# Kernel tuning notes

Hardware: AMD Instinct MI355X
Metric: run time of the kernel (lower is better)

The kernel has to match this reference:

```python
import jax, jax.numpy as jnp
import numpy as np

B, T, E = 1024, 200, 128
H = 64

def setup_inputs() -> dict:
    key = jax.random.key(0)
    k1, k2, k3, k4 = jax.random.split(key, 4)
    return {
        "query": jax.random.normal(k1, (B, 1, E), dtype=jnp.float32),
        "keys": jax.random.normal(k2, (B, T, E), dtype=jnp.float32),
        "W0": jax.random.normal(k3, (4 * E, H), dtype=jnp.float32) * 0.05,
        "b0": jnp.zeros((H,), dtype=jnp.float32),
        "W1": jax.random.normal(k4, (H, 1), dtype=jnp.float32) * 0.05,
        "b1": jnp.zeros((1,), dtype=jnp.float32),
    }

def reference(query, keys, W0, b0, W1, b1):
    # query: [B,1,E] broadcast to [B,T,E] (repeat_elements along axis 1)
    q = jnp.broadcast_to(query, keys.shape)
    # dnn_input: [B,T,4E] = concat([q, k, q-k, q*k])
    x = jnp.concatenate([q, keys, q - keys, q * keys], axis=-1)
    # one hidden layer with relu, then linear scorer -> [B,T,1]
    h = jax.nn.relu(jnp.einsum('btd,dh->bth', x, W0) + b0)
    att_score = jnp.einsum('bth,ho->bto', h, W1) + b1
    return att_score
```

## Files before the change

### kernel.cpp

```cpp
#include <hip/hip_runtime.h>
#include <hip/hip_bf16.h>


#define TB 200
#define EB 128
#define HB 64
#define KROW 136
#define KROWS 208

typedef __attribute__((ext_vector_type(8))) short bf16x8;
typedef __attribute__((ext_vector_type(4))) float f32x4;

__global__ __launch_bounds__(512, 4)
void lau_kernel(const float* __restrict__ query,
                const float* __restrict__ keys,
                const float* __restrict__ W0,
                const float* __restrict__ b0,
                const float* __restrict__ W1,
                const float* __restrict__ b1,
                float* __restrict__ out)
{
    const int b    = blockIdx.x;
    const int tid  = threadIdx.x;
    const int lane = tid & 63;
    const int wave = tid >> 6;
    const int ln15 = lane & 15;
    const int quad = lane >> 4;

    __shared__ float bias_s[HB];
    __shared__ float w1_s[HB];
    __shared__ __align__(16) unsigned char smem[KROWS * KROW * 2];

    float* q_s   = (float*)smem;
    float* red_s = (float*)(smem + 512);
    __hip_bfloat16 (*wbt)[KROW] = (__hip_bfloat16(*)[KROW])(smem + 2560);
    __hip_bfloat16 (*kt)[KROW]  = (__hip_bfloat16(*)[KROW])smem;

    const float* kb = keys + (size_t)b * TB * EB;

    if (tid < EB) q_s[tid] = query[(size_t)b * EB + tid];
    __syncthreads();

    {
        const int h     = tid & 63;
        const int chunk = tid >> 6;
        float biasp = 0.f;
        #pragma unroll 8
        for (int i = 0; i < 16; ++i) {
            const int e = chunk * 16 + i;
            const float qe  = q_s[e];
            const float w0a = W0[(size_t)e            * HB + h];
            const float w0b = W0[(size_t)(EB + e)     * HB + h];
            const float w0c = W0[(size_t)(2 * EB + e) * HB + h];
            const float w0d = W0[(size_t)(3 * EB + e) * HB + h];
            wbt[h][e] = __float2bfloat16(w0b - w0c + qe * w0d);
            biasp += qe * (w0a + w0c);
        }
        red_s[tid] = biasp;
    }
    __syncthreads();
    if (tid < HB) {
        float s = b0[tid];
        #pragma unroll
        for (int j = 0; j < 8; ++j) s += red_s[tid + 64 * j];
        bias_s[tid] = s;
        w1_s[tid]   = W1[tid];
    }
    __syncthreads();

    f32x4 g[7];
    #pragma unroll
    for (int j = 0; j < 7; ++j) {
        const int u = tid + j * 512;
        if (u < 3200) g[j] = __builtin_nontemporal_load((const f32x4*)(kb + (size_t)u * 4));
    }

    bf16x8 wbf[4][4];
    #pragma unroll
    for (int nt = 0; nt < 4; ++nt)
        #pragma unroll
        for (int ks = 0; ks < 4; ++ks)
            wbf[nt][ks] = *(const bf16x8*)&wbt[nt * 16 + ln15][quad * 8 + ks * 32];
    float w1q[4], biasq[4];
    #pragma unroll
    for (int nt = 0; nt < 4; ++nt) {
        w1q[nt]   = w1_s[nt * 16 + ln15];
        biasq[nt] = bias_s[nt * 16 + ln15];
    }

    __syncthreads();

    #pragma unroll
    for (int j = 0; j < 7; ++j) {
        const int u = tid + j * 512;
        if (u < 3200) {
            const int row  = u >> 5;
            const int col4 = (u & 31) * 4;
            union { uint2 w; __hip_bfloat162 h2[2]; } pk;
            pk.h2[0] = __float22bfloat162_rn(make_float2(g[j][0], g[j][1]));
            pk.h2[1] = __float22bfloat162_rn(make_float2(g[j][2], g[j][3]));
            *(uint2*)&kt[row][col4] = pk.w;
        }
    }
    #pragma unroll
    for (int j = 0; j < 7; ++j) {
        const int u = 3200 + tid + j * 512;
        if (u < 6400) g[j] = __builtin_nontemporal_load((const f32x4*)(kb + (size_t)u * 4));
    }
    #pragma unroll
    for (int j = 0; j < 7; ++j) {
        const int u = 3200 + tid + j * 512;
        if (u < 6400) {
            const int row  = u >> 5;
            const int col4 = (u & 31) * 4;
            union { uint2 w; __hip_bfloat162 h2[2]; } pk;
            pk.h2[0] = __float22bfloat162_rn(make_float2(g[j][0], g[j][1]));
            pk.h2[1] = __float22bfloat162_rn(make_float2(g[j][2], g[j][3]));
            *(uint2*)&kt[row][col4] = pk.w;
        }
    }
    __syncthreads();

    const float b1v = b1[0];
    for (int mt = wave; mt < 13; mt += 8) {
        bf16x8 af[4];
        #pragma unroll
        for (int ks = 0; ks < 4; ++ks)
            af[ks] = *(const bf16x8*)&kt[mt * 16 + ln15][quad * 8 + ks * 32];

        f32x4 acc[4] = {{0,0,0,0},{0,0,0,0},{0,0,0,0},{0,0,0,0}};
        #pragma unroll
        for (int ks = 0; ks < 4; ++ks)
            #pragma unroll
            for (int nt = 0; nt < 4; ++nt)
                acc[nt] = __builtin_amdgcn_mfma_f32_16x16x32_bf16(af[ks], wbf[nt][ks], acc[nt], 0, 0, 0);

        float part[4];
        #pragma unroll
        for (int r = 0; r < 4; ++r) {
            float s = 0.f;
            #pragma unroll
            for (int nt = 0; nt < 4; ++nt) {
                float hv = acc[nt][r] + biasq[nt];
                hv = hv > 0.f ? hv : 0.f;
                s += hv * w1q[nt];
            }
            part[r] = s;
        }
        #pragma unroll
        for (int m = 1; m < 16; m <<= 1) {
            #pragma unroll
            for (int r = 0; r < 4; ++r)
                part[r] += __shfl_xor(part[r], m, 64);
        }
        if (ln15 == 0) {
            #pragma unroll
            for (int r = 0; r < 4; ++r) {
                const int mg = mt * 16 + quad * 4 + r;
                if (mg < TB) out[(size_t)b * TB + mg] = part[r] + b1v;
            }
        }
    }
}

extern "C" void kernel_launch(void* const* d_in, const int* in_sizes, int n_in,
                              void* d_out, int out_size, void* d_ws, size_t ws_size,
                              hipStream_t stream) {
    const float* query = (const float*)d_in[0];
    const float* keys  = (const float*)d_in[1];
    const float* W0    = (const float*)d_in[2];
    const float* b0    = (const float*)d_in[3];
    const float* W1    = (const float*)d_in[4];
    const float* b1    = (const float*)d_in[5];
    float* out = (float*)d_out;

    lau_kernel<<<1024, 512, 0, stream>>>(query, keys, W0, b0, W1, b1, out);
}
```

Baseline: 162.8 us.

## Split weight prep into separate kernel and process two batches per block with prefetch

Moves the per-batch folding of W0 into a prep kernel. It writes a batch-independent bf16 weight matrix [W0b-W0c ; W0d] and a per-batch bias to workspace. The main kernel then computes q*k on the fly as a second K=128 MFMA pass, so the contraction grows from 128 to 256. Each block now handles two batches in half-tiles with register prefetch of the next half, which overlaps key loads with MFMA work and shrinks shared memory. The cost is double the MFMA work, a second kernel launch, and reading weight fragments from LDS inside the loop instead of keeping them in registers.

```diff
diff --git a/kernel.cpp b/kernel.cpp
--- a/kernel.cpp
+++ b/kernel.cpp
@@ -6,159 +6,204 @@
 #define EB 128
 #define HB 64
 #define KROW 136
-#define KROWS 208
+#define KT_ROWS 112
+#define WCOL 264
+#define UNITS_B 6400
+#define U_H1 3584
 
 typedef __attribute__((ext_vector_type(8))) short bf16x8;
 typedef __attribute__((ext_vector_type(4))) float f32x4;
 
+__global__ __launch_bounds__(256, 4)
+void prep_kernel(const float* __restrict__ query,
+                 const float* __restrict__ W0,
+                 const float* __restrict__ b0,
+                 unsigned char* __restrict__ ws)
+{
+    const int bid = blockIdx.x, tid = threadIdx.x;
+    __hip_bfloat16* wcat_g = (__hip_bfloat16*)ws;
+    float* bias_g = (float*)(ws + 34048);
+
+    if (bid < 64) {
+        __shared__ float p2s[EB][HB];
+        const int h = tid & 63, ec = tid >> 6;
+        #pragma unroll 4
+        for (int i = 0; i < 32; ++i) {
+            const int e = ec * 32 + i;
+            p2s[e][h] = W0[(size_t)e * HB + h] + W0[(size_t)(2 * EB + e) * HB + h];
+        }
+        __syncthreads();
+        const float b0h = b0[h];
+        for (int pass = 0; pass < 4; ++pass) {
+            const int b = bid * 16 + (tid >> 6) + pass * 4;
+            const float* q = query + (size_t)b * EB;
+            float acc = b0h;
+            #pragma unroll 8
+            for (int e = 0; e < EB; ++e) acc += q[e] * p2s[e][h];
+            bias_g[(size_t)b * HB + h] = acc;
+        }
+    } else {
+        const int h  = tid & 63;
+        const int kc = (bid - 64) * 4 + (tid >> 6);
+        float v;
+        if (kc < 128) v = W0[(size_t)(EB + kc) * HB + h] - W0[(size_t)(2 * EB + kc) * HB + h];
+        else          v = W0[(size_t)(3 * EB + (kc - 128)) * HB + h];
+        wcat_g[(size_t)h * WCOL + kc] = __float2bfloat16(v);
+    }
+}
+
 __global__ __launch_bounds__(512, 4)
-void lau_kernel(const float* __restrict__ query,
-                const float* __restrict__ keys,
-                const float* __restrict__ W0,
-                const float* __restrict__ b0,
-                const float* __restrict__ W1,
-                const float* __restrict__ b1,
-                float* __restrict__ out)
+void lau_main(const float* __restrict__ query,
+              const float* __restrict__ keys,
+              const float* __restrict__ W1,
+              const float* __restrict__ b1,
+              const unsigned char* __restrict__ ws,
+              float* __restrict__ out)
 {
-    const int b    = blockIdx.x;
-    const int tid  = threadIdx.x;
-    const int lane = tid & 63;
-    const int wave = tid >> 6;
-    const int ln15 = lane & 15;
-    const int quad = lane >> 4;
-
+    const int bid  = blockIdx.x, tid = threadIdx.x;
+    const int lane = tid & 63, wave = tid >> 6;
+    const int ln15 = lane & 15, quad = lane >> 4;
+
+    __shared__ __align__(16) __hip_bfloat16 wcat_s[HB][WCOL];
+    __shared__ __align__(16) __hip_bfloat16 kt[KT_ROWS][KROW];
+    __shared__ float q_s[EB];
     __shared__ float bias_s[HB];
     __shared__ float w1_s[HB];
-    __shared__ __align__(16) unsigned char smem[KROWS * KROW * 2];
-
-    float* q_s   = (float*)smem;
-    float* red_s = (float*)(smem + 512);
-    __hip_bfloat16 (*wbt)[KROW] = (__hip_bfloat16(*)[KROW])(smem + 2560);
-    __hip_bfloat16 (*kt)[KROW]  = (__hip_bfloat16(*)[KROW])smem;
-
+
+    const __hip_bfloat16* wcat_g = (const __hip_bfloat16*)ws;
+    const float* bias_g = (const float*)(ws + 34048);
+    const float b1v = b1[0];
+
+    int b = bid * 2;
     const float* kb = keys + (size_t)b * TB * EB;
 
-    if (tid < EB) q_s[tid] = query[(size_t)b * EB + tid];
-    __syncthreads();
+    f32x4 g[7];
+    #pragma unroll
+    for (int j = 0; j < 7; ++j)
+        g[j] = __builtin_nontemporal_load((const f32x4*)(kb + (size_t)(tid + j * 512) * 4));
 
     {
-        const int h     = tid & 63;
-        const int chunk = tid >> 6;
-        float biasp = 0.f;
-        #pragma unroll 8
-        for (int i = 0; i < 16; ++i) {
-            const int e = chunk * 16 + i;
-            const float qe  = q_s[e];
-            const float w0a = W0[(size_t)e            * HB + h];
-            const float w0b = W0[(size_t)(EB + e)     * HB + h];
-            const float w0c = W0[(size_t)(2 * EB + e) * HB + h];
-            const float w0d = W0[(size_t)(3 * EB + e) * HB + h];
-            wbt[h][e] = __float2bfloat16(w0b - w0c + qe * w0d);
-            biasp += qe * (w0a + w0c);
-        }
-        red_s[tid] = biasp;
+        const uint4* src = (const uint4*)wcat_g;
+        uint4* dst = (uint4*)&wcat_s[0][0];
+        #pragma unroll
+        for (int j = 0; j < 4; ++j) dst[tid + j * 512] = src[tid + j * 512];
+        if (tid < 64) dst[2048 + tid] = src[2048 + tid];
+        if (tid < EB) q_s[tid] = query[(size_t)b * EB + tid];
+        if (tid < HB) { bias_s[tid] = bias_g[(size_t)b * HB + tid]; w1_s[tid] = W1[tid]; }
     }
     __syncthreads();
-    if (tid < HB) {
-        float s = b0[tid];
-        #pragma unroll
-        for (int j = 0; j < 8; ++j) s += red_s[tid + 64 * j];
-        bias_s[tid] = s;
-        w1_s[tid]   = W1[tid];
-    }
-    __syncthreads();
-
-    f32x4 g[7];
+
+    float w1q[4];
     #pragma unroll
-    for (int j = 0; j < 7; ++j) {
-        const int u = tid + j * 512;
-        if (u < 3200) g[j] = __builtin_nontemporal_load((const f32x4*)(kb + (size_t)u * 4));
-    }
-
-    bf16x8 wbf[4][4];
-    #pragma unroll
-    for (int nt = 0; nt < 4; ++nt)
+    for (int nt = 0; nt < 4; ++nt) w1q[nt] = w1_s[nt * 16 + ln15];
+
+    float biasq[4];
+
+    auto do_tile = [&](int mt, int lrow) {
+        bf16x8 ak[4];
         #pragma unroll
         for (int ks = 0; ks < 4; ++ks)
-            wbf[nt][ks] = *(const bf16x8*)&wbt[nt * 16 + ln15][quad * 8 + ks * 32];
-    float w1q[4], biasq[4];
-    #pragma unroll
-    for (int nt = 0; nt < 4; ++nt) {
-        w1q[nt]   = w1_s[nt * 16 + ln15];
-        biasq[nt] = bias_s[nt * 16 + ln15];
-    }
-
-    __syncthreads();
-
-    #pragma unroll
-    for (int j = 0; j < 7; ++j) {
-        const int u = tid + j * 512;
-        if (u < 3200) {
-            const int row  = u >> 5;
-            const int col4 = (u & 31) * 4;
+            ak[ks] = *(const bf16x8*)&kt[lrow][quad * 8 + ks * 32];
+        f32x4 acc[4] = {{0,0,0,0},{0,0,0,0},{0,0,0,0},{0,0,0,0}};
+        #pragma unroll
+        for (int ks = 0; ks < 4; ++ks) {
+            #pragma unroll
+            for (int nt = 0; nt < 4; ++nt) {
+                const bf16x8 bf = *(const bf16x8*)&wcat_s[nt * 16 + ln15][quad * 8 + ks * 32];
+                acc[nt] = __builtin_amdgcn_mfma_f32_16x16x32_bf16(ak[ks], bf, acc[nt], 0, 0, 0);
+            }
+        }
+        #pragma unroll
+        for (int ks = 0; ks < 4; ++ks) {
+            union { bf16x8 v; __hip_bfloat162 h2[4]; } kk, qq;
+            kk.v = ak[ks];
+            #pragma unroll
+            for (int j = 0; j < 4; ++j) {
+                const float2 kf = __bfloat1622float2(kk.h2[j]);
+                const int e = quad * 8 + ks * 32 + 2 * j;
+                qq.h2[j] = __float22bfloat162_rn(make_float2(kf.x * q_s[e], kf.y * q_s[e + 1]));
+            }
+            #pragma unroll
+            for (int nt = 0; nt < 4; ++nt) {
+                const bf16x8 bf = *(const bf16x8*)&wcat_s[nt * 16 + ln15][128 + quad * 8 + ks * 32];
+                acc[nt] = __builtin_amdgcn_mfma_f32_16x16x32_bf16(qq.v, bf, acc[nt], 0, 0, 0);
+            }
+        }
+        float part[4];
+        #pragma unroll
+        for (int r = 0; r < 4; ++r) {
+            float s = 0.f;
+            #pragma unroll
+            for (int nt = 0; nt < 4; ++nt) {
+                float hv = acc[nt][r] + biasq[nt];
+                hv = hv > 0.f ? hv : 0.f;
+                s += hv * w1q[nt];
+            }
+            part[r] = s;
+        }
+        #pragma unroll
+        for (int m = 1; m < 16; m <<= 1) {
+            #pragma unroll
+            for (int r = 0; r < 4; ++r) part[r] += __shfl_xor(part[r], m, 64);
+        }
+        if (ln15 == 0) {
+            #pragma unroll
+            for (int r = 0; r < 4; ++r) {
+                const int mg = mt * 16 + quad * 4 + r;
+                if (mg < TB) out[(size_t)b * TB + mg] = part[r] + b1v;
+            }
+        }
+    };
+
+    for (int bt = 0; bt < 2; ++bt) {
+        #pragma unroll
+        for (int j = 0; j < 7; ++j) {
+            const int u = tid + j * 512;
+            const int row = u >> 5, col4 = (u & 31) * 4;
             union { uint2 w; __hip_bfloat162 h2[2]; } pk;
             pk.h2[0] = __float22bfloat162_rn(make_float2(g[j][0], g[j][1]));
             pk.h2[1] = __float22bfloat162_rn(make_float2(g[j][2], g[j][3]));
             *(uint2*)&kt[row][col4] = pk.w;
         }
-    }
-    #pragma unroll
-    for (int j = 0; j < 7; ++j) {
-        const int u = 3200 + tid + j * 512;
-        if (u < 6400) g[j] = __builtin_nontemporal_load((const f32x4*)(kb + (size_t)u * 4));
-    }
-    #pragma unroll
-    for (int j = 0; j < 7; ++j) {
-        const int u = 3200 + tid + j * 512;
-        if (u < 6400) {
-            const int row  = u >> 5;
-            const int col4 = (u & 31) * 4;
+        #pragma unroll
+        for (int j = 0; j < 6; ++j) {
+            int gu = U_H1 + tid + j * 512;
+            gu = gu < UNITS_B ? gu : UNITS_B - 1;
+            g[j] = __builtin_nontemporal_load((const f32x4*)(kb + (size_t)gu * 4));
+        }
+        __syncthreads();
+
+        #pragma unroll
+        for (int nt = 0; nt < 4; ++nt) biasq[nt] = bias_s[nt * 16 + ln15];
+
+        if (wave < 7) do_tile(wave, wave * 16 + ln15);
+        __syncthreads();
+
+        #pragma unroll
+        for (int j = 0; j < 6; ++j) {
+            const int u = tid + j * 512;
+            const int row = u >> 5, col4 = (u & 31) * 4;
             union { uint2 w; __hip_bfloat162 h2[2]; } pk;
             pk.h2[0] = __float22bfloat162_rn(make_float2(g[j][0], g[j][1]));
             pk.h2[1] = __float22bfloat162_rn(make_float2(g[j][2], g[j][3]));
             *(uint2*)&kt[row][col4] = pk.w;
         }
-    }
-    __syncthreads();
-
-    const float b1v = b1[0];
-    for (int mt = wave; mt < 13; mt += 8) {
-        bf16x8 af[4];
-        #pragma unroll
-        for (int ks = 0; ks < 4; ++ks)
-            af[ks] = *(const bf16x8*)&kt[mt * 16 + ln15][quad * 8 + ks * 32];
-
-        f32x4 acc[4] = {{0,0,0,0},{0,0,0,0},{0,0,0,0},{0,0,0,0}};
-        #pragma unroll
-        for (int ks = 0; ks < 4; ++ks)
-            #pragma unroll
-            for (int nt = 0; nt < 4; ++nt)
-                acc[nt] = __builtin_amdgcn_mfma_f32_16x16x32_bf16(af[ks], wbf[nt][ks], acc[nt], 0, 0, 0);
-
-        float part[4];
-        #pragma unroll
-        for (int r = 0; r < 4; ++r) {
-            float s = 0.f;
-            #pragma unroll
-            for (int nt = 0; nt < 4; ++nt) {
-                float hv = acc[nt][r] + biasq[nt];
-                hv = hv > 0.f ? hv : 0.f;
-                s += hv * w1q[nt];
-            }
-            part[r] = s;
-        }
-        #pragma unroll
-        for (int m = 1; m < 16; m <<= 1) {
-            #pragma unroll
-            for (int r = 0; r < 4; ++r)
-                part[r] += __shfl_xor(part[r], m, 64);
-        }
-        if (ln15 == 0) {
-            #pragma unroll
-            for (int r = 0; r < 4; ++r) {
-                const int mg = mt * 16 + quad * 4 + r;
-                if (mg < TB) out[(size_t)b * TB + mg] = part[r] + b1v;
-            }
+        if (bt == 0) {
+            const float* kb1 = keys + (size_t)(b + 1) * TB * EB;
+            #pragma unroll
+            for (int j = 0; j < 7; ++j)
+                g[j] = __builtin_nontemporal_load((const f32x4*)(kb1 + (size_t)(tid + j * 512) * 4));
+        }
+        __syncthreads();
+
+        if (wave < 6) do_tile(7 + wave, (7 + wave) * 16 - 112 + ln15);
+        __syncthreads();
+
+        if (bt == 0) {
+            b += 1;
+            kb = keys + (size_t)b * TB * EB;
+            if (tid < EB) q_s[tid] = query[(size_t)b * EB + tid];
+            if (tid < HB) bias_s[tid] = bias_g[(size_t)b * HB + tid];
         }
     }
 }
@@ -173,6 +218,8 @@
     const float* W1    = (const float*)d_in[4];
     const float* b1    = (const float*)d_in[5];
     float* out = (float*)d_out;
-
-    lau_kernel<<<1024, 512, 0, stream>>>(query, keys, W0, b0, W1, b1, out);
+    unsigned char* ws = (unsigned char*)d_ws;
+
+    prep_kernel<<<128, 256, 0, stream>>>(query, W0, b0, ws);
+    lau_main<<<512, 512, 0, stream>>>(query, keys, W1, b1, ws, out);
 }
```

After: 176.7 us. +8.5%, slower.

## Split per-batch weight folding into a separate prep kernel via workspace

Applied to the files above, without the earlier changes.

Moves the query-dependent folding of W0 into a bf16 weight matrix and bias into a separate prep kernel. Each prep block loads its W0 slice into registers once and reuses it across four batches, writing the results to workspace. The score kernel then reads its folded weights and bias from global memory instead of computing them, which removes the W0 loads and two barriers from its prologue. The cost is an extra launch and about 16 MB of workspace traffic, written by one kernel and read back by the next.

```diff
diff --git a/kernel.cpp b/kernel.cpp
--- a/kernel.cpp
+++ b/kernel.cpp
@@ -7,18 +7,75 @@
 #define HB 64
 #define KROW 136
 #define KROWS 208
+#define WB_BYTES (HB * EB * 2)
+#define BIAS_OFF (1024 * WB_BYTES)
 
 typedef __attribute__((ext_vector_type(8))) short bf16x8;
 typedef __attribute__((ext_vector_type(4))) float f32x4;
 
+__global__ __launch_bounds__(512, 2)
+void prep_kernel(const float* __restrict__ query,
+                 const float* __restrict__ W0,
+                 const float* __restrict__ b0,
+                 unsigned char* __restrict__ ws)
+{
+    const int bid = blockIdx.x, tid = threadIdx.x;
+    const int h     = tid & 63;
+    const int chunk = tid >> 6;
+
+    __shared__ float q_s[4][EB];
+    __shared__ float red_s[512];
+
+    for (int j = tid; j < 4 * EB; j += 512) {
+        const int bb = bid * 4 + (j >> 7);
+        q_s[j >> 7][j & 127] = query[(size_t)bb * EB + (j & 127)];
+    }
+
+    float w0a[16], w0b[16], w0c[16], w0d[16];
+    #pragma unroll
+    for (int i = 0; i < 16; ++i) {
+        const int e = chunk * 16 + i;
+        w0a[i] = W0[(size_t)e            * HB + h];
+        w0b[i] = W0[(size_t)(EB + e)     * HB + h];
+        w0c[i] = W0[(size_t)(2 * EB + e) * HB + h];
+        w0d[i] = W0[(size_t)(3 * EB + e) * HB + h];
+    }
+    __syncthreads();
+
+    const float b0h = b0[h];
+    for (int bt = 0; bt < 4; ++bt) {
+        const int b = bid * 4 + bt;
+        __hip_bfloat16* wb_g = (__hip_bfloat16*)(ws + (size_t)b * WB_BYTES);
+        float biasp = 0.f;
+        __hip_bfloat16 wbv[16];
+        #pragma unroll
+        for (int i = 0; i < 16; ++i) {
+            const int e = chunk * 16 + i;
+            const float qe = q_s[bt][e];
+            wbv[i] = __float2bfloat16(w0b[i] - w0c[i] + qe * w0d[i]);
+            biasp += qe * (w0a[i] + w0c[i]);
+        }
+        *(uint4*)&wb_g[(size_t)h * EB + chunk * 16]     = *(uint4*)&wbv[0];
+        *(uint4*)&wb_g[(size_t)h * EB + chunk * 16 + 8] = *(uint4*)&wbv[8];
+
+        red_s[tid] = biasp;
+        __syncthreads();
+        if (tid < HB) {
+            float s = b0h;
+            #pragma unroll
+            for (int j = 0; j < 8; ++j) s += red_s[tid + 64 * j];
+            ((float*)(ws + BIAS_OFF))[(size_t)b * HB + tid] = s;
+        }
+        __syncthreads();
+    }
+}
+
 __global__ __launch_bounds__(512, 4)
-void lau_kernel(const float* __restrict__ query,
-                const float* __restrict__ keys,
-                const float* __restrict__ W0,
-                const float* __restrict__ b0,
-                const float* __restrict__ W1,
-                const float* __restrict__ b1,
-                float* __restrict__ out)
+void score_kernel(const float* __restrict__ keys,
+                  const float* __restrict__ W1,
+                  const float* __restrict__ b1,
+                  const unsigned char* __restrict__ ws,
+                  float* __restrict__ out)
 {
     const int b    = blockIdx.x;
     const int tid  = threadIdx.x;
@@ -27,46 +84,9 @@
     const int ln15 = lane & 15;
     const int quad = lane >> 4;
 
-    __shared__ float bias_s[HB];
-    __shared__ float w1_s[HB];
-    __shared__ __align__(16) unsigned char smem[KROWS * KROW * 2];
-
-    float* q_s   = (float*)smem;
-    float* red_s = (float*)(smem + 512);
-    __hip_bfloat16 (*wbt)[KROW] = (__hip_bfloat16(*)[KROW])(smem + 2560);
-    __hip_bfloat16 (*kt)[KROW]  = (__hip_bfloat16(*)[KROW])smem;
+    __shared__ __align__(16) __hip_bfloat16 kt[KROWS][KROW];
 
     const float* kb = keys + (size_t)b * TB * EB;
-
-    if (tid < EB) q_s[tid] = query[(size_t)b * EB + tid];
-    __syncthreads();
-
-    {
-        const int h     = tid & 63;
-        const int chunk = tid >> 6;
-        float biasp = 0.f;
-        #pragma unroll 8
-        for (int i = 0; i < 16; ++i) {
-            const int e = chunk * 16 + i;
-            const float qe  = q_s[e];
-            const float w0a = W0[(size_t)e            * HB + h];
-            const float w0b = W0[(size_t)(EB + e)     * HB + h];
-            const float w0c = W0[(size_t)(2 * EB + e) * HB + h];
-            const float w0d = W0[(size_t)(3 * EB + e) * HB + h];
-            wbt[h][e] = __float2bfloat16(w0b - w0c + qe * w0d);
-            biasp += qe * (w0a + w0c);
-        }
-        red_s[tid] = biasp;
-    }
-    __syncthreads();
-    if (tid < HB) {
-        float s = b0[tid];
-        #pragma unroll
-        for (int j = 0; j < 8; ++j) s += red_s[tid + 64 * j];
-        bias_s[tid] = s;
-        w1_s[tid]   = W1[tid];
-    }
-    __syncthreads();
 
     f32x4 g[7];
     #pragma unroll
@@ -75,27 +95,25 @@
         if (u < 3200) g[j] = __builtin_nontemporal_load((const f32x4*)(kb + (size_t)u * 4));
     }
 
+    const __hip_bfloat16* wb_g = (const __hip_bfloat16*)(ws + (size_t)b * WB_BYTES);
     bf16x8 wbf[4][4];
     #pragma unroll
     for (int nt = 0; nt < 4; ++nt)
         #pragma unroll
         for (int ks = 0; ks < 4; ++ks)
-            wbf[nt][ks] = *(const bf16x8*)&wbt[nt * 16 + ln15][quad * 8 + ks * 32];
+            wbf[nt][ks] = *(const bf16x8*)&wb_g[(size_t)(nt * 16 + ln15) * EB + quad * 8 + ks * 32];
     float w1q[4], biasq[4];
     #pragma unroll
     for (int nt = 0; nt < 4; ++nt) {
-        w1q[nt]   = w1_s[nt * 16 + ln15];
-        biasq[nt] = bias_s[nt * 16 + ln15];
+        w1q[nt]   = W1[nt * 16 + ln15];
+        biasq[nt] = ((const float*)(ws + BIAS_OFF))[(size_t)b * HB + nt * 16 + ln15];
     }
-
-    __syncthreads();
 
     #pragma unroll
     for (int j = 0; j < 7; ++j) {
         const int u = tid + j * 512;
         if (u < 3200) {
-            const int row  = u >> 5;
-            const int col4 = (u & 31) * 4;
+            const int row = u >> 5, col4 = (u & 31) * 4;
             union { uint2 w; __hip_bfloat162 h2[2]; } pk;
             pk.h2[0] = __float22bfloat162_rn(make_float2(g[j][0], g[j][1]));
             pk.h2[1] = __float22bfloat162_rn(make_float2(g[j][2], g[j][3]));
@@ -111,8 +129,7 @@
     for (int j = 0; j < 7; ++j) {
         const int u = 3200 + tid + j * 512;
         if (u < 6400) {
-            const int row  = u >> 5;
-            const int col4 = (u & 31) * 4;
+            const int row = u >> 5, col4 = (u & 31) * 4;
             union { uint2 w; __hip_bfloat162 h2[2]; } pk;
             pk.h2[0] = __float22bfloat162_rn(make_float2(g[j][0], g[j][1]));
             pk.h2[1] = __float22bfloat162_rn(make_float2(g[j][2], g[j][3]));
@@ -173,6 +190,8 @@
     const float* W1    = (const float*)d_in[4];
     const float* b1    = (const float*)d_in[5];
     float* out = (float*)d_out;
+    unsigned char* ws = (unsigned char*)d_ws;
 
-    lau_kernel<<<1024, 512, 0, stream>>>(query, keys, W0, b0, W1, b1, out);
+    prep_kernel<<<256, 512, 0, stream>>>(query, W0, b0, ws);
+    score_kernel<<<1024, 512, 0, stream>>>(keys, W1, b1, ws, out);
 }
```

New measurement: 170.5 us. 1.05x slower.

## Give keys and weights separate LDS and issue all key loads in one batch

Applied to the files above, without the earlier changes.

Replaces the aliased shared-memory buffer with separate arrays for query, reduction, weights and keys. This removes the sync that separated weight-fragment reads from key staging. All 13 key loads per thread are now issued in one batch, with clamped indices instead of guards, right after the bias reduction, so more global memory traffic is in flight before the single barrier. Weight fragments are re-read from LDS inside the MFMA loop rather than held in registers. This lowers register pressure but adds LDS traffic, and the larger LDS footprint may reduce blocks per CU.

```diff
diff --git a/kernel.cpp b/kernel.cpp
--- a/kernel.cpp
+++ b/kernel.cpp
@@ -7,6 +7,7 @@
 #define HB 64
 #define KROW 136
 #define KROWS 208
+#define UNITS_B 6400
 
 typedef __attribute__((ext_vector_type(8))) short bf16x8;
 typedef __attribute__((ext_vector_type(4))) float f32x4;
@@ -27,14 +28,12 @@
     const int ln15 = lane & 15;
     const int quad = lane >> 4;
 
+    __shared__ float q_s[EB];
+    __shared__ float red_s[512];
     __shared__ float bias_s[HB];
     __shared__ float w1_s[HB];
-    __shared__ __align__(16) unsigned char smem[KROWS * KROW * 2];
-
-    float* q_s   = (float*)smem;
-    float* red_s = (float*)(smem + 512);
-    __hip_bfloat16 (*wbt)[KROW] = (__hip_bfloat16(*)[KROW])(smem + 2560);
-    __hip_bfloat16 (*kt)[KROW]  = (__hip_bfloat16(*)[KROW])smem;
+    __shared__ __align__(16) __hip_bfloat16 wbt[HB][KROW];
+    __shared__ __align__(16) __hip_bfloat16 kt[KROWS][KROW];
 
     const float* kb = keys + (size_t)b * TB * EB;
 
@@ -66,62 +65,35 @@
         bias_s[tid] = s;
         w1_s[tid]   = W1[tid];
     }
+
+    f32x4 g[13];
+    #pragma unroll
+    for (int j = 0; j < 13; ++j) {
+        int u = tid + j * 512;
+        u = u < UNITS_B ? u : UNITS_B - 1;
+        g[j] = __builtin_nontemporal_load((const f32x4*)(kb + (size_t)u * 4));
+    }
+    #pragma unroll
+    for (int j = 0; j < 13; ++j) {
+        int u = tid + j * 512;
+        u = u < UNITS_B ? u : UNITS_B - 1;
+        const int row = u >> 5, col4 = (u & 31) * 4;
+        union { uint2 w; __hip_bfloat162 h2[2]; } pk;
+        pk.h2[0] = __float22bfloat162_rn(make_float2(g[j][0], g[j][1]));
+        pk.h2[1] = __float22bfloat162_rn(make_float2(g[j][2], g[j][3]));
+        *(uint2*)&kt[row][col4] = pk.w;
+    }
     __syncthreads();
 
-    f32x4 g[7];
-    #pragma unroll
-    for (int j = 0; j < 7; ++j) {
-        const int u = tid + j * 512;
-        if (u < 3200) g[j] = __builtin_nontemporal_load((const f32x4*)(kb + (size_t)u * 4));
-    }
-
-    bf16x8 wbf[4][4];
-    #pragma unroll
-    for (int nt = 0; nt < 4; ++nt)
-        #pragma unroll
-        for (int ks = 0; ks < 4; ++ks)
-            wbf[nt][ks] = *(const bf16x8*)&wbt[nt * 16 + ln15][quad * 8 + ks * 32];
+    const __hip_bfloat16* wb_base = &wbt[ln15][quad * 8];
     float w1q[4], biasq[4];
     #pragma unroll
     for (int nt = 0; nt < 4; ++nt) {
         w1q[nt]   = w1_s[nt * 16 + ln15];
         biasq[nt] = bias_s[nt * 16 + ln15];
     }
+    const float b1v = b1[0];
 
-    __syncthreads();
-
-    #pragma unroll
-    for (int j = 0; j < 7; ++j) {
-        const int u = tid + j * 512;
-        if (u < 3200) {
-            const int row  = u >> 5;
-            const int col4 = (u & 31) * 4;
-            union { uint2 w; __hip_bfloat162 h2[2]; } pk;
-            pk.h2[0] = __float22bfloat162_rn(make_float2(g[j][0], g[j][1]));
-            pk.h2[1] = __float22bfloat162_rn(make_float2(g[j][2], g[j][3]));
-            *(uint2*)&kt[row][col4] = pk.w;
-        }
-    }
-    #pragma unroll
-    for (int j = 0; j < 7; ++j) {
-        const int u = 3200 + tid + j * 512;
-        if (u < 6400) g[j] = __builtin_nontemporal_load((const f32x4*)(kb + (size_t)u * 4));
-    }
-    #pragma unroll
-    for (int j = 0; j < 7; ++j) {
-        const int u = 3200 + tid + j * 512;
-        if (u < 6400) {
-            const int row  = u >> 5;
-            const int col4 = (u & 31) * 4;
-            union { uint2 w; __hip_bfloat162 h2[2]; } pk;
-            pk.h2[0] = __float22bfloat162_rn(make_float2(g[j][0], g[j][1]));
-            pk.h2[1] = __float22bfloat162_rn(make_float2(g[j][2], g[j][3]));
-            *(uint2*)&kt[row][col4] = pk.w;
-        }
-    }
-    __syncthreads();
-
-    const float b1v = b1[0];
     for (int mt = wave; mt < 13; mt += 8) {
         bf16x8 af[4];
         #pragma unroll
@@ -132,8 +104,10 @@
         #pragma unroll
         for (int ks = 0; ks < 4; ++ks)
             #pragma unroll
-            for (int nt = 0; nt < 4; ++nt)
-                acc[nt] = __builtin_amdgcn_mfma_f32_16x16x32_bf16(af[ks], wbf[nt][ks], acc[nt], 0, 0, 0);
+            for (int nt = 0; nt < 4; ++nt) {
+                const bf16x8 bf = *(const bf16x8*)(wb_base + nt * 16 * KROW + ks * 32);
+                acc[nt] = __builtin_amdgcn_mfma_f32_16x16x32_bf16(af[ks], bf, acc[nt], 0, 0, 0);
+            }
 
         float part[4];
         #pragma unroll
```

Measured after the change: 162.8 us. Within noise of the previous version (-0.0%).
